# Kernel tuning notes

Measured on AMD Instinct MI355X. Metric: run time of the kernel, lower is better.

## Reference

```python
import jax, jax.numpy as jnp
import numpy as np

DIM = 256
WIN = 7
HEADS = 8
N = WIN * WIN
HEAD_DIM = DIM // HEADS
SCALE = HEAD_DIM ** -0.5


def _relative_position_index():
    coords = np.stack(np.meshgrid(np.arange(WIN), np.arange(WIN), indexing='ij'))  # [2,W,W]
    cf = coords.reshape(2, -1)  # [2, N]
    rel = cf[:, :, None] - cf[:, None, :]  # [2, N, N]
    rel = rel.transpose(1, 2, 0)  # [N, N, 2]
    rel[:, :, 0] += WIN - 1
    rel[:, :, 1] += WIN - 1
    rel[:, :, 0] *= 2 * WIN - 1
    return rel.sum(-1).astype(np.int32)  # [N, N]


def setup_inputs() -> dict:
    key = jax.random.key(0)
    ks = jax.random.split(key, 8)
    B_ = 4096
    nW = 64
    x = jax.random.normal(ks[0], (B_, N, DIM), dtype=jnp.float32)
    mask = jnp.zeros((nW, N, N), dtype=jnp.float32)
    qkv_w = jax.random.normal(ks[1], (3 * DIM, DIM), dtype=jnp.float32) * (DIM ** -0.5)
    qkv_b = jnp.zeros((3 * DIM,), dtype=jnp.float32)
    proj_w = jax.random.normal(ks[2], (DIM, DIM), dtype=jnp.float32) * (DIM ** -0.5)
    proj_b = jnp.zeros((DIM,), dtype=jnp.float32)
    bias_table = jax.random.normal(ks[3], ((2 * WIN - 1) ** 2, HEADS), dtype=jnp.float32) * 0.02
    rel_index = jnp.asarray(_relative_position_index())
    return {"x": x, "mask": mask, "qkv_w": qkv_w, "qkv_b": qkv_b,
            "proj_w": proj_w, "proj_b": proj_b, "bias_table": bias_table,
            "rel_index": rel_index}


def reference(x, mask, qkv_w, qkv_b, proj_w, proj_b, bias_table, rel_index):
    B_, n, C = x.shape
    qkv = (x @ qkv_w.T + qkv_b).reshape(B_, n, 3, HEADS, HEAD_DIM)
    qkv = qkv.transpose(2, 0, 3, 1, 4)  # [3, B_, H, N, d]
    q, k, v = qkv[0], qkv[1], qkv[2]
    attn = jnp.einsum('bhnd,bhmd->bhnm', q * SCALE, k)  # [B_, H, N, N]
    # gather relative position bias: [N*N] -> [N, N, H] -> [H, N, N]
    bias = bias_table[rel_index.reshape(-1)].reshape(n, n, HEADS).transpose(2, 0, 1)
    attn = attn + bias[None]
    nW = mask.shape[0]
    attn = attn.reshape(B_ // nW, nW, HEADS, n, n) + mask[None, :, None]
    attn = jax.nn.softmax(attn.reshape(B_, HEADS, n, n), axis=-1)
    out = jnp.einsum('bhnm,bhmd->bhnd', attn, v)
    out = out.transpose(0, 2, 1, 3).reshape(B_, n, C)
    return out @ proj_w.T + proj_b
```

## Files before the change

kernel.cpp:

```cpp
#include <hip/hip_runtime.h>

#define NTOK 49
#define NW   64
#define SCALEQ 0.17677669529663687f

typedef __bf16 bf16;
typedef __bf16 bf16x4 __attribute__((ext_vector_type(4)));
typedef __bf16 bf16x8 __attribute__((ext_vector_type(8)));
typedef float  f32x4  __attribute__((ext_vector_type(4)));

#define QS_OFF   0
#define KS_OFF   15680
#define VTS_OFF  31360
#define UN_OFF   45696
#define P_STRIDE 3528
#define SMEM_ELEMS 73920
#define SMEM_BYTES (SMEM_ELEMS*2)
static_assert(SMEM_BYTES == 147840, "lds budget");

__global__ __launch_bounds__(256) void prep_kernel(
    const float* __restrict__ qkv_w, const float* __restrict__ proj_w,
    const float* __restrict__ bias_table, const int* __restrict__ rel_index,
    bf16* __restrict__ wq, bf16* __restrict__ wp, float* __restrict__ bias_full)
{
  int i = blockIdx.x * 256 + threadIdx.x;
  if (i < 768*256) wq[i] = (bf16)qkv_w[i];
  if (i < 256*256) wp[i] = (bf16)proj_w[i];
  if (i < 8*49*49) {
    int h  = i / 2401;
    int nm = i - h*2401;
    bias_full[i] = bias_table[rel_index[nm]*8 + h];
  }
}

__global__ void __launch_bounds__(1024)
win_attn_kernel(const float* __restrict__ x,
                const float* __restrict__ mask,
                const float* __restrict__ qkv_b,
                const float* __restrict__ proj_b,
                const bf16*  __restrict__ wq,
                const bf16*  __restrict__ wp,
                const float* __restrict__ bias_full,
                float* __restrict__ out)
{
  extern __shared__ bf16 smem[];
  const int b    = blockIdx.x;
  const int tid  = threadIdx.x;
  const int wave = tid >> 6;
  const int lane = tid & 63;
  const int quad = lane >> 4;
  const int l16  = lane & 15;
  const int w    = b & (NW - 1);

  bf16* qs  = smem + QS_OFF;
  bf16* ks  = smem + KS_OFF;
  bf16* vts = smem + VTS_OFF;
  bf16* xs  = smem + UN_OFF;

  f32x4 zero4 = {0.f, 0.f, 0.f, 0.f};

  {
    const float4* xv = (const float4*)(x + (size_t)b * (NTOK*256));
    for (int i = tid; i < NTOK*64; i += 1024) {
      float4 v = xv[i];
      int n = i >> 6, c = (i & 63) * 4;
      bf16x4 pk = {(bf16)v.x, (bf16)v.y, (bf16)v.z, (bf16)v.w};
      *(bf16x4*)(xs + n*264 + c) = pk;
    }
    for (int i = tid; i < 8*32*7; i += 1024) {
      int h = i / 224, r = i - h*224;
      int dd = r / 7, mm = 49 + (r - dd*7);
      vts[(h*32 + dd)*56 + mm] = (bf16)0.0f;
    }
  }
  __syncthreads();

  {
    f32x4 acc[3][4];
#pragma unroll
    for (int t = 0; t < 3; ++t)
#pragma unroll
      for (int tr = 0; tr < 4; ++tr) acc[t][tr] = zero4;

    int jc0 = (wave*3)*16 + l16;
    const bf16* w0 = wq + (size_t)jc0*256 + quad*8;
#pragma unroll
    for (int kk = 0; kk < 8; ++kk) {
      bf16x8 afr[4];
#pragma unroll
      for (int tr = 0; tr < 4; ++tr) {
        int m = tr*16 + l16; if (m > 48) m = 48;
        afr[tr] = *(const bf16x8*)(xs + m*264 + quad*8 + kk*32);
      }
#pragma unroll
      for (int t = 0; t < 3; ++t) {
        bf16x8 bfr = *(const bf16x8*)(w0 + (size_t)t*16*256 + kk*32);
#pragma unroll
        for (int tr = 0; tr < 4; ++tr)
          acc[t][tr] = __builtin_amdgcn_mfma_f32_16x16x32_bf16(afr[tr], bfr, acc[t][tr], 0,0,0);
      }
    }
#pragma unroll
    for (int t = 0; t < 3; ++t) {
      int jcol = (wave*3 + t)*16 + l16;
      float bj = qkv_b[jcol];
      int s  = jcol >> 8;
      int hh = (jcol >> 5) & 7;
      int dd = jcol & 31;
#pragma unroll
      for (int tr = 0; tr < 4; ++tr) {
#pragma unroll
        for (int rg = 0; rg < 4; ++rg) {
          int row = tr*16 + quad*4 + rg;
          if (row < 49) {
            float v = acc[t][tr][rg] + bj;
            if (s == 0)      qs[(hh*49 + row)*40 + dd] = (bf16)(v * SCALEQ);
            else if (s == 1) ks[(hh*49 + row)*40 + dd] = (bf16)v;
            else             vts[(hh*32 + dd)*56 + row] = (bf16)v;
          }
        }
      }
    }
  }
  __syncthreads();

  f32x4 O[2][2];
  {
    const int h    = wave >> 1;
    const int half = wave & 1;
    const bf16* qh = qs  + h*49*40;
    const bf16* kh = ks  + h*49*40;
    const bf16* vh = vts + h*32*56;
    bf16* Pb = smem + UN_OFF + h * P_STRIDE;

    bf16x8 qf[2], kf[4];
#pragma unroll
    for (int t = 0; t < 2; ++t) {
      int m = (half*2 + t)*16 + l16; if (m > 48) m = 48;
      qf[t] = *(const bf16x8*)(qh + m*40 + quad*8);
    }
#pragma unroll
    for (int t = 0; t < 4; ++t) {
      int m = t*16 + l16; if (m > 48) m = 48;
      kf[t] = *(const bf16x8*)(kh + m*40 + quad*8);
    }
    f32x4 S[2][4];
#pragma unroll
    for (int tr = 0; tr < 2; ++tr)
#pragma unroll
      for (int tc = 0; tc < 4; ++tc)
        S[tr][tc] = __builtin_amdgcn_mfma_f32_16x16x32_bf16(qf[tr], kf[tc], zero4, 0,0,0);

    const float* bh = bias_full + h*2401;
    const float* mw = mask + w*2401;
#pragma unroll
    for (int tr2 = 0; tr2 < 2; ++tr2) {
      int tr = half*2 + tr2;
#pragma unroll
      for (int rg = 0; rg < 4; ++rg) {
        int row = tr*16 + quad*4 + rg;
#pragma unroll
        for (int tc = 0; tc < 4; ++tc) {
          int col = tc*16 + l16;
          float v = S[tr2][tc][rg];
          if (col >= 49) v = -1e30f;
          else if (row < 49) {
            int idx = row*49 + col;
            v += bh[idx] + mw[idx];
          }
          S[tr2][tc][rg] = v;
        }
        float mx = fmaxf(fmaxf(S[tr2][0][rg], S[tr2][1][rg]),
                         fmaxf(S[tr2][2][rg], S[tr2][3][rg]));
#pragma unroll
        for (int off = 1; off < 16; off <<= 1)
          mx = fmaxf(mx, __shfl_xor(mx, off));
        float sum = 0.f;
#pragma unroll
        for (int tc = 0; tc < 4; ++tc) {
          float p = __expf(S[tr2][tc][rg] - mx);
          S[tr2][tc][rg] = p;
          sum += p;
        }
#pragma unroll
        for (int off = 1; off < 16; off <<= 1)
          sum += __shfl_xor(sum, off);
        float inv = 1.f / sum;
        if (row < 49) {
#pragma unroll
          for (int tc = 0; tc < 4; ++tc)
            Pb[row*72 + tc*16 + l16] = (bf16)(S[tr2][tc][rg] * inv);
        }
      }
    }

#pragma unroll
    for (int tr = 0; tr < 2; ++tr) { O[tr][0] = zero4; O[tr][1] = zero4; }
#pragma unroll
    for (int kst = 0; kst < 2; ++kst) {
      int mc  = kst*32 + quad*8;
      int mcv = (mc >= 56) ? 0 : mc;
      bf16x8 vf0 = *(const bf16x8*)(vh + l16*56 + mcv);
      bf16x8 vf1 = *(const bf16x8*)(vh + (16 + l16)*56 + mcv);
#pragma unroll
      for (int tr2 = 0; tr2 < 2; ++tr2) {
        int row = (half*2 + tr2)*16 + l16; if (row > 48) row = 48;
        bf16x8 pf = *(const bf16x8*)(Pb + row*72 + mc);
        O[tr2][0] = __builtin_amdgcn_mfma_f32_16x16x32_bf16(pf, vf0, O[tr2][0], 0,0,0);
        O[tr2][1] = __builtin_amdgcn_mfma_f32_16x16x32_bf16(pf, vf1, O[tr2][1], 0,0,0);
      }
    }
  }
  __syncthreads();

  bf16* ost = smem + UN_OFF;
  {
    const int h    = wave >> 1;
    const int half = wave & 1;
#pragma unroll
    for (int tr2 = 0; tr2 < 2; ++tr2)
#pragma unroll
      for (int rg = 0; rg < 4; ++rg) {
        int row = (half*2 + tr2)*16 + quad*4 + rg;
        if (row < 49) {
          ost[row*264 + h*32 + l16]      = (bf16)O[tr2][0][rg];
          ost[row*264 + h*32 + 16 + l16] = (bf16)O[tr2][1][rg];
        }
      }
  }
  __syncthreads();

  {
    f32x4 acc[4];
#pragma unroll
    for (int tr = 0; tr < 4; ++tr) acc[tr] = zero4;
    int ocol = wave*16 + l16;
    const bf16* wrow = wp + (size_t)ocol*256 + quad*8;
#pragma unroll
    for (int kk = 0; kk < 8; ++kk) {
      bf16x8 bfr = *(const bf16x8*)(wrow + kk*32);
#pragma unroll
      for (int tr = 0; tr < 4; ++tr) {
        int m = tr*16 + l16; if (m > 48) m = 48;
        bf16x8 afr = *(const bf16x8*)(ost + m*264 + quad*8 + kk*32);
        acc[tr] = __builtin_amdgcn_mfma_f32_16x16x32_bf16(afr, bfr, acc[tr], 0,0,0);
      }
    }
    float bj = proj_b[ocol];
    float* ob = out + (size_t)b * (NTOK*256);
#pragma unroll
    for (int tr = 0; tr < 4; ++tr)
#pragma unroll
      for (int rg = 0; rg < 4; ++rg) {
        int row = tr*16 + quad*4 + rg;
        if (row < 49) ob[row*256 + ocol] = acc[tr][rg] + bj;
      }
  }
}

extern "C" void kernel_launch(void* const* d_in, const int* in_sizes, int n_in,
                              void* d_out, int out_size, void* d_ws, size_t ws_size,
                              hipStream_t stream) {
  const float* x          = (const float*)d_in[0];
  const float* mask       = (const float*)d_in[1];
  const float* qkv_w      = (const float*)d_in[2];
  const float* qkv_b      = (const float*)d_in[3];
  const float* proj_w     = (const float*)d_in[4];
  const float* proj_b     = (const float*)d_in[5];
  const float* bias_table = (const float*)d_in[6];
  const int*   rel_index  = (const int*)d_in[7];
  float* out = (float*)d_out;

  bf16*  wq        = (bf16*)d_ws;
  bf16*  wp        = wq + 768*256;
  float* bias_full = (float*)((char*)d_ws + 524288);

  prep_kernel<<<768, 256, 0, stream>>>(qkv_w, proj_w, bias_table, rel_index,
                                       wq, wp, bias_full);

  (void)hipFuncSetAttribute(reinterpret_cast<const void*>(&win_attn_kernel),
                            hipFuncAttributeMaxDynamicSharedMemorySize, SMEM_BYTES);
  win_attn_kernel<<<4096, 1024, SMEM_BYTES, stream>>>(
      x, mask, qkv_b, proj_b, wq, wp, bias_full, out);
}
```

Before: 737.0 us.

## Split heads into two groups per block to halve LDS and raise occupancy

The block size drops from 1024 to 512 threads and the 8 heads are processed in two passes of 4. Each pass computes the QKV projection only for its head group, and the P matrix reuses the Q/K buffer after a barrier. This roughly halves LDS per block so that two blocks can be resident per CU instead of one, improving latency hiding. In exchange it adds barriers, keeps the O accumulators for both groups live in registers, and reads the x tile twice.

```diff
diff --git a/kernel.cpp b/kernel.cpp
--- a/kernel.cpp
+++ b/kernel.cpp
@@ -9,14 +9,15 @@
 typedef __bf16 bf16x8 __attribute__((ext_vector_type(8)));
 typedef float  f32x4  __attribute__((ext_vector_type(4)));
 
-#define QS_OFF   0
-#define KS_OFF   15680
-#define VTS_OFF  31360
-#define UN_OFF   45696
-#define P_STRIDE 3528
-#define SMEM_ELEMS 73920
+#define QK_OFF  0
+#define QK_H    3920
+#define K_SUB   1960
+#define P_LD    72
+#define VTS_OFF 15680
+#define XS_OFF  22848
+#define SMEM_ELEMS 35784
 #define SMEM_BYTES (SMEM_ELEMS*2)
-static_assert(SMEM_BYTES == 147840, "lds budget");
+static_assert(SMEM_BYTES == 71568, "lds budget");
 
 __global__ __launch_bounds__(256) void prep_kernel(
     const float* __restrict__ qkv_w, const float* __restrict__ proj_w,
@@ -33,7 +34,7 @@
   }
 }
 
-__global__ void __launch_bounds__(1024)
+__global__ void __launch_bounds__(512, 4)
 win_attn_kernel(const float* __restrict__ x,
                 const float* __restrict__ mask,
                 const float* __restrict__ qkv_b,
@@ -52,209 +53,239 @@
   const int l16  = lane & 15;
   const int w    = b & (NW - 1);
 
-  bf16* qs  = smem + QS_OFF;
-  bf16* ks  = smem + KS_OFF;
+  bf16* qk  = smem + QK_OFF;
   bf16* vts = smem + VTS_OFF;
-  bf16* xs  = smem + UN_OFF;
+  bf16* xs  = smem + XS_OFF;
 
   f32x4 zero4 = {0.f, 0.f, 0.f, 0.f};
 
   {
     const float4* xv = (const float4*)(x + (size_t)b * (NTOK*256));
-    for (int i = tid; i < NTOK*64; i += 1024) {
+    for (int i = tid; i < NTOK*64; i += 512) {
       float4 v = xv[i];
       int n = i >> 6, c = (i & 63) * 4;
       bf16x4 pk = {(bf16)v.x, (bf16)v.y, (bf16)v.z, (bf16)v.w};
       *(bf16x4*)(xs + n*264 + c) = pk;
     }
-    for (int i = tid; i < 8*32*7; i += 1024) {
-      int h = i / 224, r = i - h*224;
+    for (int i = tid; i < 4*32*7; i += 512) {
+      int hh = i / 224, r = i - hh*224;
       int dd = r / 7, mm = 49 + (r - dd*7);
-      vts[(h*32 + dd)*56 + mm] = (bf16)0.0f;
+      vts[(hh*32 + dd)*56 + mm] = (bf16)0.0f;
     }
   }
   __syncthreads();
 
+  const int hl   = wave >> 1;
+  const int half = wave & 1;
+
+  f32x4 O[2][2][2];
+
+#pragma unroll 2
+  for (int hg = 0; hg < 2; ++hg) {
+    {
+      f32x4 acc[3][4];
+#pragma unroll
+      for (int t = 0; t < 3; ++t)
+#pragma unroll
+        for (int tr = 0; tr < 4; ++tr) acc[t][tr] = zero4;
+
+      const bf16* wrow[3];
+      int jc_[3], s_[3], tl_[3];
+#pragma unroll
+      for (int t = 0; t < 3; ++t) {
+        int tt = wave*3 + t;
+        s_[t]  = tt >> 3;
+        tl_[t] = tt & 7;
+        jc_[t] = s_[t]*256 + hg*128 + tl_[t]*16 + l16;
+        wrow[t] = wq + (size_t)jc_[t]*256 + quad*8;
+      }
+#pragma unroll
+      for (int kk = 0; kk < 8; ++kk) {
+        bf16x8 afr[4];
+#pragma unroll
+        for (int tr = 0; tr < 4; ++tr) {
+          int m = tr*16 + l16; if (m > 48) m = 48;
+          afr[tr] = *(const bf16x8*)(xs + m*264 + quad*8 + kk*32);
+        }
+#pragma unroll
+        for (int t = 0; t < 3; ++t) {
+          bf16x8 bfr = *(const bf16x8*)(wrow[t] + kk*32);
+#pragma unroll
+          for (int tr = 0; tr < 4; ++tr)
+            acc[t][tr] = __builtin_amdgcn_mfma_f32_16x16x32_bf16(afr[tr], bfr, acc[t][tr], 0,0,0);
+        }
+      }
+#pragma unroll
+      for (int t = 0; t < 3; ++t) {
+        float bj = qkv_b[jc_[t]];
+        int hh = tl_[t] >> 1;
+        int dd = jc_[t] & 31;
+#pragma unroll
+        for (int tr = 0; tr < 4; ++tr)
+#pragma unroll
+          for (int rg = 0; rg < 4; ++rg) {
+            int row = tr*16 + quad*4 + rg;
+            if (row < 49) {
+              float v = acc[t][tr][rg] + bj;
+              if (s_[t] == 0)      qk[hh*QK_H + row*40 + dd] = (bf16)(v * SCALEQ);
+              else if (s_[t] == 1) qk[hh*QK_H + K_SUB + row*40 + dd] = (bf16)v;
+              else                 vts[(hh*32 + dd)*56 + row] = (bf16)v;
+            }
+          }
+      }
+    }
+    __syncthreads();
+
+    {
+      const int h = hg*4 + hl;
+      const bf16* qh = qk  + hl*QK_H;
+      const bf16* kh = qh + K_SUB;
+      const bf16* vh = vts + hl*(32*56);
+      bf16* Pb = qk + hl*QK_H;
+
+      bf16x8 qf[2], kf[4];
+#pragma unroll
+      for (int t = 0; t < 2; ++t) {
+        int m = (half*2 + t)*16 + l16; if (m > 48) m = 48;
+        qf[t] = *(const bf16x8*)(qh + m*40 + quad*8);
+      }
+#pragma unroll
+      for (int t = 0; t < 4; ++t) {
+        int m = t*16 + l16; if (m > 48) m = 48;
+        kf[t] = *(const bf16x8*)(kh + m*40 + quad*8);
+      }
+      __syncthreads();
+
+      f32x4 S[2][4];
+#pragma unroll
+      for (int tr = 0; tr < 2; ++tr)
+#pragma unroll
+        for (int tc = 0; tc < 4; ++tc)
+          S[tr][tc] = __builtin_amdgcn_mfma_f32_16x16x32_bf16(qf[tr], kf[tc], zero4, 0,0,0);
+
+      const float* bh = bias_full + h*2401;
+      const float* mw = mask + w*2401;
+#pragma unroll
+      for (int tr2 = 0; tr2 < 2; ++tr2) {
+        int tr = half*2 + tr2;
+#pragma unroll
+        for (int rg = 0; rg < 4; ++rg) {
+          int row = tr*16 + quad*4 + rg;
+#pragma unroll
+          for (int tc = 0; tc < 4; ++tc) {
+            int col = tc*16 + l16;
+            float v = S[tr2][tc][rg];
+            if (col >= 49) v = -1e30f;
+            else if (row < 49) {
+              int idx = row*49 + col;
+              v += bh[idx] + mw[idx];
+            }
+            S[tr2][tc][rg] = v;
+          }
+          float mx = fmaxf(fmaxf(S[tr2][0][rg], S[tr2][1][rg]),
+                           fmaxf(S[tr2][2][rg], S[tr2][3][rg]));
+#pragma unroll
+          for (int off = 1; off < 16; off <<= 1)
+            mx = fmaxf(mx, __shfl_xor(mx, off));
+          float sum = 0.f;
+#pragma unroll
+          for (int tc = 0; tc < 4; ++tc) {
+            float p = __expf(S[tr2][tc][rg] - mx);
+            S[tr2][tc][rg] = p;
+            sum += p;
+          }
+#pragma unroll
+          for (int off = 1; off < 16; off <<= 1)
+            sum += __shfl_xor(sum, off);
+          float inv = 1.f / sum;
+          if (row < 49) {
+#pragma unroll
+            for (int tc = 0; tc < 4; ++tc)
+              Pb[row*P_LD + tc*16 + l16] = (bf16)(S[tr2][tc][rg] * inv);
+          }
+        }
+      }
+
+      O[hg][0][0] = zero4; O[hg][0][1] = zero4;
+      O[hg][1][0] = zero4; O[hg][1][1] = zero4;
+#pragma unroll
+      for (int kst = 0; kst < 2; ++kst) {
+        int mc  = kst*32 + quad*8;
+        int mcv = (mc >= 56) ? 0 : mc;
+        bf16x8 vf0 = *(const bf16x8*)(vh + l16*56 + mcv);
+        bf16x8 vf1 = *(const bf16x8*)(vh + (16 + l16)*56 + mcv);
+#pragma unroll
+        for (int tr2 = 0; tr2 < 2; ++tr2) {
+          int row = (half*2 + tr2)*16 + l16; if (row > 48) row = 48;
+          bf16x8 pf = *(const bf16x8*)(Pb + row*P_LD + mc);
+          O[hg][tr2][0] = __builtin_amdgcn_mfma_f32_16x16x32_bf16(pf, vf0, O[hg][tr2][0], 0,0,0);
+          O[hg][tr2][1] = __builtin_amdgcn_mfma_f32_16x16x32_bf16(pf, vf1, O[hg][tr2][1], 0,0,0);
+        }
+      }
+    }
+    __syncthreads();
+  }
+
+  bf16* ost = smem;
   {
-    f32x4 acc[3][4];
-#pragma unroll
-    for (int t = 0; t < 3; ++t)
+#pragma unroll 2
+    for (int hg = 0; hg < 2; ++hg) {
+      int h = hg*4 + hl;
+#pragma unroll
+      for (int tr2 = 0; tr2 < 2; ++tr2)
+#pragma unroll
+        for (int rg = 0; rg < 4; ++rg) {
+          int row = (half*2 + tr2)*16 + quad*4 + rg;
+          if (row < 49) {
+            ost[row*264 + h*32 + l16]      = (bf16)O[hg][tr2][0][rg];
+            ost[row*264 + h*32 + 16 + l16] = (bf16)O[hg][tr2][1][rg];
+          }
+        }
+    }
+  }
+  __syncthreads();
+
+  {
+    f32x4 acc[2][4];
+#pragma unroll
+    for (int t = 0; t < 2; ++t)
 #pragma unroll
       for (int tr = 0; tr < 4; ++tr) acc[t][tr] = zero4;
-
-    int jc0 = (wave*3)*16 + l16;
-    const bf16* w0 = wq + (size_t)jc0*256 + quad*8;
+    int oc[2];
+    const bf16* wrow[2];
+#pragma unroll
+    for (int t = 0; t < 2; ++t) {
+      oc[t] = (wave*2 + t)*16 + l16;
+      wrow[t] = wp + (size_t)oc[t]*256 + quad*8;
+    }
 #pragma unroll
     for (int kk = 0; kk < 8; ++kk) {
       bf16x8 afr[4];
 #pragma unroll
       for (int tr = 0; tr < 4; ++tr) {
         int m = tr*16 + l16; if (m > 48) m = 48;
-        afr[tr] = *(const bf16x8*)(xs + m*264 + quad*8 + kk*32);
-      }
-#pragma unroll
-      for (int t = 0; t < 3; ++t) {
-        bf16x8 bfr = *(const bf16x8*)(w0 + (size_t)t*16*256 + kk*32);
+        afr[tr] = *(const bf16x8*)(ost + m*264 + quad*8 + kk*32);
+      }
+#pragma unroll
+      for (int t = 0; t < 2; ++t) {
+        bf16x8 bfr = *(const bf16x8*)(wrow[t] + kk*32);
 #pragma unroll
         for (int tr = 0; tr < 4; ++tr)
           acc[t][tr] = __builtin_amdgcn_mfma_f32_16x16x32_bf16(afr[tr], bfr, acc[t][tr], 0,0,0);
       }
     }
-#pragma unroll
-    for (int t = 0; t < 3; ++t) {
-      int jcol = (wave*3 + t)*16 + l16;
-      float bj = qkv_b[jcol];
-      int s  = jcol >> 8;
-      int hh = (jcol >> 5) & 7;
-      int dd = jcol & 31;
-#pragma unroll
-      for (int tr = 0; tr < 4; ++tr) {
+    float* ob = out + (size_t)b * (NTOK*256);
+#pragma unroll
+    for (int t = 0; t < 2; ++t) {
+      float bj = proj_b[oc[t]];
+#pragma unroll
+      for (int tr = 0; tr < 4; ++tr)
 #pragma unroll
         for (int rg = 0; rg < 4; ++rg) {
           int row = tr*16 + quad*4 + rg;
-          if (row < 49) {
-            float v = acc[t][tr][rg] + bj;
-            if (s == 0)      qs[(hh*49 + row)*40 + dd] = (bf16)(v * SCALEQ);
-            else if (s == 1) ks[(hh*49 + row)*40 + dd] = (bf16)v;
-            else             vts[(hh*32 + dd)*56 + row] = (bf16)v;
-          }
-        }
-      }
-    }
-  }
-  __syncthreads();
-
-  f32x4 O[2][2];
-  {
-    const int h    = wave >> 1;
-    const int half = wave & 1;
-    const bf16* qh = qs  + h*49*40;
-    const bf16* kh = ks  + h*49*40;
-    const bf16* vh = vts + h*32*56;
-    bf16* Pb = smem + UN_OFF + h * P_STRIDE;
-
-    bf16x8 qf[2], kf[4];
-#pragma unroll
-    for (int t = 0; t < 2; ++t) {
-      int m = (half*2 + t)*16 + l16; if (m > 48) m = 48;
-      qf[t] = *(const bf16x8*)(qh + m*40 + quad*8);
-    }
-#pragma unroll
-    for (int t = 0; t < 4; ++t) {
-      int m = t*16 + l16; if (m > 48) m = 48;
-      kf[t] = *(const bf16x8*)(kh + m*40 + quad*8);
-    }
-    f32x4 S[2][4];
-#pragma unroll
-    for (int tr = 0; tr < 2; ++tr)
-#pragma unroll
-      for (int tc = 0; tc < 4; ++tc)
-        S[tr][tc] = __builtin_amdgcn_mfma_f32_16x16x32_bf16(qf[tr], kf[tc], zero4, 0,0,0);
-
-    const float* bh = bias_full + h*2401;
-    const float* mw = mask + w*2401;
-#pragma unroll
-    for (int tr2 = 0; tr2 < 2; ++tr2) {
-      int tr = half*2 + tr2;
-#pragma unroll
-      for (int rg = 0; rg < 4; ++rg) {
-        int row = tr*16 + quad*4 + rg;
-#pragma unroll
-        for (int tc = 0; tc < 4; ++tc) {
-          int col = tc*16 + l16;
-          float v = S[tr2][tc][rg];
-          if (col >= 49) v = -1e30f;
-          else if (row < 49) {
-            int idx = row*49 + col;
-            v += bh[idx] + mw[idx];
-          }
-          S[tr2][tc][rg] = v;
-        }
-        float mx = fmaxf(fmaxf(S[tr2][0][rg], S[tr2][1][rg]),
-                         fmaxf(S[tr2][2][rg], S[tr2][3][rg]));
-#pragma unroll
-        for (int off = 1; off < 16; off <<= 1)
-          mx = fmaxf(mx, __shfl_xor(mx, off));
-        float sum = 0.f;
-#pragma unroll
-        for (int tc = 0; tc < 4; ++tc) {
-          float p = __expf(S[tr2][tc][rg] - mx);
-          S[tr2][tc][rg] = p;
-          sum += p;
-        }
-#pragma unroll
-        for (int off = 1; off < 16; off <<= 1)
-          sum += __shfl_xor(sum, off);
-        float inv = 1.f / sum;
-        if (row < 49) {
-#pragma unroll
-          for (int tc = 0; tc < 4; ++tc)
-            Pb[row*72 + tc*16 + l16] = (bf16)(S[tr2][tc][rg] * inv);
-        }
-      }
-    }
-
-#pragma unroll
-    for (int tr = 0; tr < 2; ++tr) { O[tr][0] = zero4; O[tr][1] = zero4; }
-#pragma unroll
-    for (int kst = 0; kst < 2; ++kst) {
-      int mc  = kst*32 + quad*8;
-      int mcv = (mc >= 56) ? 0 : mc;
-      bf16x8 vf0 = *(const bf16x8*)(vh + l16*56 + mcv);
-      bf16x8 vf1 = *(const bf16x8*)(vh + (16 + l16)*56 + mcv);
-#pragma unroll
-      for (int tr2 = 0; tr2 < 2; ++tr2) {
-        int row = (half*2 + tr2)*16 + l16; if (row > 48) row = 48;
-        bf16x8 pf = *(const bf16x8*)(Pb + row*72 + mc);
-        O[tr2][0] = __builtin_amdgcn_mfma_f32_16x16x32_bf16(pf, vf0, O[tr2][0], 0,0,0);
-        O[tr2][1] = __builtin_amdgcn_mfma_f32_16x16x32_bf16(pf, vf1, O[tr2][1], 0,0,0);
-      }
-    }
-  }
-  __syncthreads();
-
-  bf16* ost = smem + UN_OFF;
-  {
-    const int h    = wave >> 1;
-    const int half = wave & 1;
-#pragma unroll
-    for (int tr2 = 0; tr2 < 2; ++tr2)
-#pragma unroll
-      for (int rg = 0; rg < 4; ++rg) {
-        int row = (half*2 + tr2)*16 + quad*4 + rg;
-        if (row < 49) {
-          ost[row*264 + h*32 + l16]      = (bf16)O[tr2][0][rg];
-          ost[row*264 + h*32 + 16 + l16] = (bf16)O[tr2][1][rg];
-        }
-      }
-  }
-  __syncthreads();
-
-  {
-    f32x4 acc[4];
-#pragma unroll
-    for (int tr = 0; tr < 4; ++tr) acc[tr] = zero4;
-    int ocol = wave*16 + l16;
-    const bf16* wrow = wp + (size_t)ocol*256 + quad*8;
-#pragma unroll
-    for (int kk = 0; kk < 8; ++kk) {
-      bf16x8 bfr = *(const bf16x8*)(wrow + kk*32);
-#pragma unroll
-      for (int tr = 0; tr < 4; ++tr) {
-        int m = tr*16 + l16; if (m > 48) m = 48;
-        bf16x8 afr = *(const bf16x8*)(ost + m*264 + quad*8 + kk*32);
-        acc[tr] = __builtin_amdgcn_mfma_f32_16x16x32_bf16(afr, bfr, acc[tr], 0,0,0);
-      }
-    }
-    float bj = proj_b[ocol];
-    float* ob = out + (size_t)b * (NTOK*256);
-#pragma unroll
-    for (int tr = 0; tr < 4; ++tr)
-#pragma unroll
-      for (int rg = 0; rg < 4; ++rg) {
-        int row = tr*16 + quad*4 + rg;
-        if (row < 49) ob[row*256 + ocol] = acc[tr][rg] + bj;
-      }
+          if (row < 49) ob[row*256 + oc[t]] = acc[t][tr][rg] + bj;
+        }
+    }
   }
 }
 
@@ -280,6 +311,6 @@
 
   (void)hipFuncSetAttribute(reinterpret_cast<const void*>(&win_attn_kernel),
                             hipFuncAttributeMaxDynamicSharedMemorySize, SMEM_BYTES);
-  win_attn_kernel<<<4096, 1024, SMEM_BYTES, stream>>>(
+  win_attn_kernel<<<4096, 512, SMEM_BYTES, stream>>>(
       x, mask, qkv_b, proj_b, wq, wp, bias_full, out);
 }
```

After: 835.6 us. 13.4% more time.
